# Kernel optimization log

Measured on AMD Instinct MI355X. Metric: run time of the kernel, lower is better.

The kernel has to match this reference:

```python
import jax, jax.numpy as jnp
import numpy as np
import math

NUM_CLASSES = 80
CENTER_RADIUS = 2.5
EPS = 1e-7
IMG = 1280.0


def _ciou(gt, pd):
    # gt: [G,4] xyxy, pd: [A,4] xyxy -> CIoU [G,A] (matches ultralytics bbox_iou, CIoU=True)
    b1 = gt[:, None, :]
    b2 = pd[None, :, :]
    iw = jnp.clip(jnp.minimum(b1[..., 2], b2[..., 2]) - jnp.maximum(b1[..., 0], b2[..., 0]), 0.0)
    ih = jnp.clip(jnp.minimum(b1[..., 3], b2[..., 3]) - jnp.maximum(b1[..., 1], b2[..., 1]), 0.0)
    inter = iw * ih
    w1 = b1[..., 2] - b1[..., 0]; h1 = b1[..., 3] - b1[..., 1]
    w2 = b2[..., 2] - b2[..., 0]; h2 = b2[..., 3] - b2[..., 1]
    union = w1 * h1 + w2 * h2 - inter + EPS
    iou = inter / union
    cw = jnp.maximum(b1[..., 2], b2[..., 2]) - jnp.minimum(b1[..., 0], b2[..., 0])
    ch = jnp.maximum(b1[..., 3], b2[..., 3]) - jnp.minimum(b1[..., 1], b2[..., 1])
    c2 = cw * cw + ch * ch + EPS
    rho2 = ((b2[..., 0] + b2[..., 2] - b1[..., 0] - b1[..., 2]) ** 2 +
            (b2[..., 1] + b2[..., 3] - b1[..., 1] - b1[..., 3]) ** 2) / 4.0
    v = (4.0 / math.pi ** 2) * (jnp.arctan(w2 / (h2 + EPS)) - jnp.arctan(w1 / (h1 + EPS))) ** 2
    alpha = v / (v - iou + (1.0 + EPS))
    return iou - (rho2 / c2 + v * alpha)


def _assign_one(scores, boxes, gt_lab, gt_box, valid, stride, anc):
    # scores [A,C], boxes [A,4], gt_lab [G], gt_box [G,4], valid [G] bool, stride [A,1], anc [A,2]
    G = gt_lab.shape[0]
    C = scores.shape[-1]
    # geometry constraint: anchor center within radius*stride of gt center
    gcx = (gt_box[:, 0] + gt_box[:, 2]) / 2.0
    gcy = (gt_box[:, 1] + gt_box[:, 3]) / 2.0
    cd = (stride[:, 0] * CENTER_RADIUS)[None, :]            # [1,A]
    in_center = (jnp.abs(anc[None, :, 0] - gcx[:, None]) < cd) & \
                (jnp.abs(anc[None, :, 1] - gcy[:, None]) < cd)
    in_center = in_center & valid[:, None]                  # [G,A]
    anchor_filter = in_center.any(axis=0)                   # [A]
    # pairwise CIoU (zeroed outside the filtered anchor set / invalid gts)
    ious = jnp.clip(_ciou(gt_box, boxes), 0.0)
    ious = ious * anchor_filter[None, :].astype(ious.dtype) * valid[:, None].astype(ious.dtype)
    iou_loss = -jnp.log(ious + 1e-8)
    # BCE(sqrt(p), onehot) summed over classes, computed without [G,A,C] tensor:
    # sum_c BCE = -sum_c log(1-p_c) - log p_{c_g} + log(1-p_{c_g})
    p = jnp.sqrt(scores)
    logp = jnp.clip(jnp.log(p), -100.0)
    log1mp = jnp.clip(jnp.log1p(-p), -100.0)
    base = -log1mp.sum(-1)                                  # [A]
    lp_g = jnp.take(logp, gt_lab, axis=1).T                 # [G,A]
    l1m_g = jnp.take(log1mp, gt_lab, axis=1).T              # [G,A]
    cls_loss = base[None, :] - lp_g + l1m_g
    # cost; extra 1e8/1e9 penalties emulate torch's exclusion of unfiltered anchors / invalid gts
    cost = (cls_loss + 3.0 * iou_loss
            + 1e6 * (~in_center).astype(cls_loss.dtype)
            + 1e8 * (~anchor_filter)[None, :].astype(cls_loss.dtype)
            + 1e9 * (~valid)[:, None].astype(cls_loss.dtype))
    # dynamic-k: sum of top-10 ious per gt
    topk_ious = jax.lax.top_k(ious, 10)[0]
    dyn_k = jnp.maximum((topk_ious.sum(-1) + 0.5).astype(jnp.int32), 1)
    # per-gt pick dyn_k lowest-cost anchors via rank
    ranks = jnp.argsort(jnp.argsort(cost, axis=-1), axis=-1)
    matching = (ranks < dyn_k[:, None]) & valid[:, None]    # [G,A] bool
    # conflict resolution: anchors matched to >1 gt keep min-cost gt
    cnt = matching.sum(0)                                   # [A]
    best_g = jnp.argmin(cost, axis=0)                       # [A]
    onehot_g = jnp.arange(G)[:, None] == best_g[None, :]
    matching = jnp.where(cnt[None, :] > 1, onehot_g, matching)
    fg = matching.any(axis=0)                               # [A]
    mg = jnp.argmax(matching, axis=0)                       # [A]
    pred_iou = (matching.astype(ious.dtype) * ious).sum(0)  # [A]
    labels = jnp.where(fg, gt_lab[mg], NUM_CLASSES).astype(jnp.int32)
    tboxes = gt_box[mg] * fg[:, None].astype(gt_box.dtype)
    tscores = jax.nn.one_hot(gt_lab[mg], C, dtype=scores.dtype) * (pred_iou * fg)[:, None]
    tgt_idx = jnp.where(fg, mg, 0).astype(jnp.int32)
    return labels, tboxes, tscores, fg, tgt_idx


def setup_inputs() -> dict:
    key = jax.random.key(0)
    ks = jax.random.split(key, 10)
    bs, A, G, C = 16, 33600, 64, NUM_CLASSES
    pd_scores = jax.random.uniform(ks[0], (bs, A, C), jnp.float32, 1e-4, 0.99)
    cxy = jax.random.uniform(ks[1], (bs, A, 2), jnp.float32, 0.0, IMG)
    wh = jax.random.uniform(ks[2], (bs, A, 2), jnp.float32, 8.0, 128.0)
    pd_bboxes = jnp.concatenate([cxy - wh / 2, cxy + wh / 2], axis=-1)
    anc_points = jax.random.uniform(ks[3], (A, 2), jnp.float32, 0.0, IMG)
    gt_labels = jax.random.randint(ks[4], (bs, G, 1), 0, C, jnp.int32)
    gcxy = jax.random.uniform(ks[5], (bs, G, 2), jnp.float32, 64.0, IMG - 64.0)
    gwh = jax.random.uniform(ks[6], (bs, G, 2), jnp.float32, 16.0, 256.0)
    gt_bboxes = jnp.concatenate([gcxy - gwh / 2, gcxy + gwh / 2], axis=-1)
    mask_gt = (jax.random.randint(ks[7], (bs, G, 1), 0, 5, jnp.int32) < 4).astype(jnp.int32)
    stride = (8.0 * (2.0 ** jax.random.randint(ks[8], (bs, A, 1), 0, 3, jnp.int32).astype(jnp.float32)))
    return {"pd_scores": pd_scores, "pd_bboxes": pd_bboxes, "anc_points": anc_points,
            "gt_labels": gt_labels, "gt_bboxes": gt_bboxes, "mask_gt": mask_gt, "stride": stride}


def reference(pd_scores, pd_bboxes, anc_points, gt_labels, gt_bboxes, mask_gt, stride):
    gt_lab = gt_labels[..., 0].astype(jnp.int32)
    valid = mask_gt[..., 0].astype(bool)
    fn = jax.vmap(_assign_one, in_axes=(0, 0, 0, 0, 0, 0, None))
    return fn(pd_scores, pd_bboxes, gt_lab, gt_bboxes, valid, stride, anc_points)
```

## Files before the change

kernel.cpp:

```cpp
#include <hip/hip_runtime.h>
#include <float.h>
#include <math.h>

#define NA 33600
#define NG 64
#define NC 80
#define NB 16
#define CRAD 2.5f
#define MCAP 12288

typedef float vfloat4 __attribute__((ext_vector_type(4)));

#define O_CNT   0ULL
#define O_AG    2150400ULL
#define O_AIOU  4300800ULL
#define O_BASE  6451200ULL
#define O_CCNT  8601600ULL
#define O_CONFC 8601664ULL
#define O_CONFL 8601728ULL
#define O_CA    8667264ULL
#define O_CBASE 9453696ULL
#define O_COLT  10240128ULL
#define WS_NEED_COLT (10240128ULL + 62914560ULL)
#define O_CPB   73154688ULL
#define O_CAP   76300416ULL
#define WS_NEED_PC (76300416ULL + 3145728ULL)
#define O_PIOU  79446144ULL
#define O_PCST  79528064ULL
#define O_PIDX  79609984ULL
#define O_CKEY  79773824ULL
#define WS_NEED_KEY (79773824ULL + 786432ULL)

#define OFF_LAB 0L
#define OFF_TB  537600L
#define OFF_TS  2688000L
#define OFF_FG  45696000L
#define OFF_TGT 46233600L
#define OUT_TOTAL 46771200L

__device__ __forceinline__ float ciou_clip(float gx1, float gy1, float gx2, float gy2,
                                           float w1, float h1, float at1, float at2v,
                                           float4 pb) {
    float iw = fmaxf(fminf(gx2, pb.z) - fmaxf(gx1, pb.x), 0.f);
    float ih = fmaxf(fminf(gy2, pb.w) - fmaxf(gy1, pb.y), 0.f);
    float inter = iw * ih;
    float w2 = pb.z - pb.x, h2 = pb.w - pb.y;
    float uni = w1 * h1 + w2 * h2 - inter + 1e-7f;
    float iou = inter / uni;
    float cw = fmaxf(gx2, pb.z) - fminf(gx1, pb.x);
    float ch = fmaxf(gy2, pb.w) - fminf(gy1, pb.y);
    float c2 = cw * cw + ch * ch + 1e-7f;
    float dx = pb.x + pb.z - gx1 - gx2;
    float dy = pb.y + pb.w - gy1 - gy2;
    float rho2 = (dx * dx + dy * dy) * 0.25f;
    float dat = at2v - at1;
    float v = 0.4052847345693511f * (dat * dat);
    float alpha = v / ((v - iou) + 1.0000001f);
    float ci = iou - (rho2 / c2 + v * alpha);
    return fmaxf(ci, 0.f);
}

__global__ __launch_bounds__(256) void k1a_cand(
    const float* __restrict__ anc, const float* __restrict__ gbox,
    const int* __restrict__ gmask, const float* __restrict__ strd,
    int* __restrict__ candA, unsigned int* __restrict__ candKey, int use_key,
    int* __restrict__ candCnt, int* __restrict__ cnt)
{
    __shared__ float2 s_c[NG];
    const int b = blockIdx.y, tid = threadIdx.x;
    if (tid < NG) {
        const float4 gb = ((const float4*)gbox)[b * NG + tid];
        const int v = gmask[b * NG + tid];
        float gcx = (gb.x + gb.z) * 0.5f;
        float gcy = (gb.y + gb.w) * 0.5f;
        s_c[tid] = make_float2(v ? gcx : 3.0e30f, gcy);
    }
    __syncthreads();
    const int a = blockIdx.x * 256 + tid;
    int f = 0;
    if (a < NA) {
        cnt[(long)b * NA + a] = 0;
        float2 ap = ((const float2*)anc)[a];
        float cd = strd[(long)b * NA + a] * CRAD;
        #pragma unroll
        for (int g = 0; g < NG; ++g) {
            float2 c = s_c[g];
            f |= (int)((fabsf(ap.x - c.x) < cd) & (fabsf(ap.y - c.y) < cd));
        }
    }
    unsigned long long m = __ballot(f);
    int lane = tid & 63;
    int wcnt = __popcll(m);
    int pre = __popcll(m & ((1ULL << lane) - 1ULL));
    int base0 = 0;
    if (lane == 0 && wcnt) base0 = atomicAdd(&candCnt[b], wcnt);
    base0 = __shfl(base0, 0, 64);
    if (f) {
        int pos = base0 + pre;
        if (pos < MCAP) {
            candA[b * MCAP + pos] = a;
            if (use_key) candKey[b * MCAP + pos] = ((unsigned int)a << 16) | (unsigned int)pos;
        }
    }
}

__global__ __launch_bounds__(256) void k1b_gather(
    const float* __restrict__ scores, const float* __restrict__ pdb,
    const float* __restrict__ anc, const float* __restrict__ strd,
    const int* __restrict__ candCnt, const int* __restrict__ candA,
    float* __restrict__ base, float* __restrict__ candBase,
    float* __restrict__ colT, int use_colT,
    float4* __restrict__ candPB, float4* __restrict__ candAp, int use_pc)
{
    __shared__ float s_l1m[64][81];
    const int b = blockIdx.y;
    int M = candCnt[b]; if (M > MCAP) M = MCAP;
    if (blockIdx.x * 64 >= M) return;
    const int q   = threadIdx.x >> 2;
    const int sub = threadIdx.x & 3;
    const int j = blockIdx.x * 64 + q;
    const bool active = (j < M);
    int a = 0;
    if (active) a = candA[b * MCAP + j];
    const long ia = (long)b * NA + a;
    if (active) {
        if (sub == 1 && use_pc) {
            float4 pb = ((const float4*)pdb)[ia];
            float2 ap = ((const float2*)anc)[a];
            float cd = strd[ia] * CRAD;
            float at2v = atanf((pb.z - pb.x) / ((pb.w - pb.y) + 1e-7f));
            candPB[b * MCAP + j] = pb;
            candAp[b * MCAP + j] = make_float4(ap.x, ap.y, cd, at2v);
        }
        const vfloat4* srow = (const vfloat4*)(scores + ia * NC);
        float* ct = colT + (long)b * NC * MCAP + j;
        #pragma unroll
        for (int qq = 0; qq < 5; ++qq) {
            vfloat4 s4 = __builtin_nontemporal_load(&srow[sub * 5 + qq]);
            float sv[4] = {s4.x, s4.y, s4.z, s4.w};
            #pragma unroll
            for (int k = 0; k < 4; ++k) {
                const int c = sub * 20 + 4 * qq + k;
                float p = sqrtf(sv[k]);
                float l1m = fmaxf(log1pf(-p), -100.f);
                s_l1m[q][c] = l1m;
                if (use_colT) {
                    float lp = fmaxf(logf(p), -100.f);
                    __builtin_nontemporal_store(l1m - lp, &ct[(long)c * MCAP]);
                }
            }
        }
    }
    __syncthreads();
    if (active && sub == 0) {
        float bsum = 0.f;
        #pragma unroll
        for (int c = 0; c < NC; ++c)
            bsum += s_l1m[q][c];
        const float bval = -bsum;
        base[ia] = bval;
        candBase[b * MCAP + j] = bval;
    }
}

__global__ __launch_bounds__(256) void k2_scan(
    const int* __restrict__ glab, const float* __restrict__ gbox,
    const int* __restrict__ gmask,
    const int* __restrict__ candCnt, const unsigned int* __restrict__ candKey,
    const float* __restrict__ candBase, const float* __restrict__ colT,
    const float4* __restrict__ candPB, const float4* __restrict__ candAp,
    float* __restrict__ partIou, float* __restrict__ partCost,
    unsigned int* __restrict__ partIdx)
{
    const int i = blockIdx.y;
    const int s = blockIdx.x;
    const int b = (i & 7) | ((i >> 9) << 3);
    const int g = (i >> 3) & 63;
    if (gmask[b * NG + g] == 0) return;
    const int tid = threadIdx.x, lane = tid & 63, wid = tid >> 6;
    __shared__ float s_v[4];
    __shared__ int s_i[4];
    __shared__ unsigned int s_u[4];

    const float4 gb = ((const float4*)gbox)[b * NG + g];
    const int lab = glab[b * NG + g];
    const float gcx = (gb.x + gb.z) * 0.5f, gcy = (gb.y + gb.w) * 0.5f;
    const float w1 = gb.z - gb.x, h1 = gb.w - gb.y;
    const float at1 = atanf(w1 / (h1 + 1e-7f));
    const int bM = b * MCAP;
    int M = candCnt[b]; if (M > MCAP) M = MCAP;
    const float* colrow = colT + (long)(b * NC + lab) * MCAP;

    float liou[10];
    float lcost[10]; unsigned int lkey[10];
    #pragma unroll
    for (int j = 0; j < 10; ++j) {
        liou[j] = 0.f;
        lcost[j] = FLT_MAX; lkey[j] = 0xFFFFFFFFu;
    }

    for (int jj = s * 256 + tid; jj < M; jj += 512) {
        const unsigned int key = candKey[bM + jj];
        const float4 pb = candPB[bM + jj];
        const float4 t  = candAp[bM + jj];
        const float cb  = candBase[bM + jj];
        const float cr  = colrow[jj];
        float ci = ciou_clip(gb.x, gb.y, gb.z, gb.w, w1, h1, at1, t.w, pb);
        bool inc = (fabsf(t.x - gcx) < t.z) && (fabsf(t.y - gcy) < t.z);
        float colv = cb + cr;
        float cost = colv + 3.0f * (-logf(ci + 1e-8f));
        if (!inc) cost += 1e6f;

        if (ci > liou[9]) {
            #pragma unroll
            for (int k = 9; k >= 1; --k) {
                bool ck   = (liou[k] > ci);
                bool ckm1 = (liou[k - 1] > ci);
                liou[k] = ck ? liou[k] : (ckm1 ? ci : liou[k - 1]);
            }
            liou[0] = (liou[0] > ci) ? liou[0] : ci;
        }
        if (cost < lcost[9] || (cost == lcost[9] && key < lkey[9])) {
            #pragma unroll
            for (int k = 9; k >= 1; --k) {
                bool ck   = (lcost[k] < cost) || (lcost[k] == cost && lkey[k] < key);
                bool ckm1 = (lcost[k - 1] < cost) || (lcost[k - 1] == cost && lkey[k - 1] < key);
                lcost[k] = ck ? lcost[k] : (ckm1 ? cost : lcost[k - 1]);
                lkey[k]  = ck ? lkey[k]  : (ckm1 ? key  : lkey[k - 1]);
            }
            bool c0 = (lcost[0] < cost) || (lcost[0] == cost && lkey[0] < key);
            lcost[0] = c0 ? lcost[0] : cost;
            lkey[0]  = c0 ? lkey[0]  : key;
        }
    }

    const int pbase = i * 20 + s * 10;
    for (int it = 0; it < 10; ++it) {
        float bv = liou[0];
        #pragma unroll
        for (int off = 32; off > 0; off >>= 1)
            bv = fmaxf(bv, __shfl_down(bv, off, 64));
        if (lane == 0) s_v[wid] = bv;
        __syncthreads();
        float wv = fmaxf(fmaxf(s_v[0], s_v[1]), fmaxf(s_v[2], s_v[3]));
        if (tid == 0) partIou[pbase + it] = wv;
        unsigned long long m = __ballot(liou[0] == wv);
        int fl = m ? (int)__ffsll((long long)m) - 1 : 64;
        if (lane == 0) s_i[wid] = fl;
        __syncthreads();
        int ow, ol;
        if (s_i[0] < 64)      { ow = 0; ol = s_i[0]; }
        else if (s_i[1] < 64) { ow = 1; ol = s_i[1]; }
        else if (s_i[2] < 64) { ow = 2; ol = s_i[2]; }
        else                  { ow = 3; ol = s_i[3]; }
        if (wid == ow && lane == ol) {
            #pragma unroll
            for (int k = 0; k < 9; ++k) liou[k] = liou[k + 1];
            liou[9] = -2.f;
        }
        __syncthreads();
    }
    for (int it = 0; it < 10; ++it) {
        float bc = lcost[0]; unsigned int bk = lkey[0];
        #pragma unroll
        for (int off = 32; off > 0; off >>= 1) {
            float oc = __shfl_down(bc, off, 64);
            unsigned int ok = __shfl_down(bk, off, 64);
            if (oc < bc || (oc == bc && ok < bk)) { bc = oc; bk = ok; }
        }
        if (lane == 0) { s_v[wid] = bc; s_u[wid] = bk; }
        __syncthreads();
        float wc = s_v[0]; unsigned int wk = s_u[0];
        #pragma unroll
        for (int w = 1; w < 4; ++w)
            if (s_v[w] < wc || (s_v[w] == wc && s_u[w] < wk)) { wc = s_v[w]; wk = s_u[w]; }
        if (lcost[0] == wc && lkey[0] == wk) {
            partCost[pbase + it] = wc;
            partIdx[pbase + it]  = wk;
            #pragma unroll
            for (int k = 0; k < 9; ++k) { lcost[k] = lcost[k + 1]; lkey[k] = lkey[k + 1]; }
            lcost[9] = FLT_MAX; lkey[9] = 0xFFFFFFFFu;
        }
        __syncthreads();
    }
}

__global__ __launch_bounds__(256) void k2b_merge(
    const int* __restrict__ gmask, const float* __restrict__ gbox,
    const float* __restrict__ partIou, const float* __restrict__ partCost,
    const unsigned int* __restrict__ partIdx,
    const float4* __restrict__ candPB, const float4* __restrict__ candAp,
    int* __restrict__ cnt, int* __restrict__ ag, float* __restrict__ aiou)
{
    const int lane = threadIdx.x & 63;
    const int wv0 = blockIdx.x * 4 + (threadIdx.x >> 6);
    for (int i = wv0; i < NB * NG; i += gridDim.x * 4) {
        const int b = (i & 7) | ((i >> 9) << 3);
        const int g = (i >> 3) & 63;
        if (gmask[b * NG + g] == 0) continue;
        float v = (lane < 20) ? partIou[i * 20 + lane] : -2.f;
        float acc = 0.f;
        for (int it = 0; it < 10; ++it) {
            float bv = v;
            #pragma unroll
            for (int off = 32; off > 0; off >>= 1)
                bv = fmaxf(bv, __shfl_down(bv, off, 64));
            bv = __shfl(bv, 0, 64);
            acc += bv;
            unsigned long long m = __ballot(v == bv);
            int first = (int)__ffsll((long long)m) - 1;
            if (lane == first) v = -3.f;
        }
        int K = (int)(acc + 0.5f);
        if (K < 1) K = 1;

        const float4 gbw = ((const float4*)gbox)[b * NG + g];
        const float w1w = gbw.z - gbw.x, h1w = gbw.w - gbw.y;
        const float at1w = atanf(w1w / (h1w + 1e-7f));
        const long bA = (long)b * NA;
        const int bM = b * MCAP;
        float c  = (lane < 20) ? partCost[i * 20 + lane] : FLT_MAX;
        unsigned int idx = (lane < 20) ? partIdx[i * 20 + lane] : 0xFFFFFFFFu;
        for (int it = 0; it < K; ++it) {
            float bc = c; unsigned int bk = idx;
            #pragma unroll
            for (int off = 32; off > 0; off >>= 1) {
                float oc = __shfl_down(bc, off, 64);
                unsigned int ok = __shfl_down(bk, off, 64);
                if (oc < bc || (oc == bc && ok < bk)) { bc = oc; bk = ok; }
            }
            bc = __shfl(bc, 0, 64);
            bk = (unsigned int)__shfl((int)bk, 0, 64);
            bool own = (c == bc && idx == bk);
            unsigned long long mo = __ballot(own);
            int fl = (int)__ffsll((long long)mo) - 1;
            if (own && lane == fl) {
                unsigned int aa = bk >> 16;
                if (aa < NA) {
                    int j = (int)(bk & 0xFFFFu);
                    float4 pbw = candPB[bM + j];
                    float4 tw  = candAp[bM + j];
                    float ciw = ciou_clip(gbw.x, gbw.y, gbw.z, gbw.w, w1w, h1w, at1w, tw.w, pbw);
                    atomicAdd(&cnt[bA + aa], 1);
                    ag[bA + aa] = g;
                    aiou[bA + aa] = ciw;
                }
            }
            if (own) { c = FLT_MAX; idx = 0xFFFFFFFFu; }
        }
    }
}

__global__ __launch_bounds__(256) void k2_select(
    const float* __restrict__ scores, const float* __restrict__ pdb,
    const float* __restrict__ anc, const int* __restrict__ glab,
    const float* __restrict__ gbox, const int* __restrict__ gmask,
    const float* __restrict__ strd,
    const int* __restrict__ candCnt, const int* __restrict__ candA,
    const float* __restrict__ candBase, const float* __restrict__ colT, int use_colT,
    const float4* __restrict__ candPB, const float4* __restrict__ candAp, int use_pc,
    int* __restrict__ cnt, int* __restrict__ ag, float* __restrict__ aiou)
{
    const int i = blockIdx.x;
    const int b = (i & 7) | ((i >> 9) << 3);
    const int g = (i >> 3) & 63;
    if (gmask[b * NG + g] == 0) return;
    const int tid = threadIdx.x, lane = tid & 63, wid = tid >> 6;
    __shared__ float s_v[4];
    __shared__ int s_i[4];

    const float4 gb = ((const float4*)gbox)[b * NG + g];
    const int lab = glab[b * NG + g];
    const float gcx = (gb.x + gb.z) * 0.5f, gcy = (gb.y + gb.w) * 0.5f;
    const float w1 = gb.z - gb.x, h1 = gb.w - gb.y;
    const float at1 = atanf(w1 / (h1 + 1e-7f));
    const long bA = (long)b * NA;
    const int bM = b * MCAP;
    int M = candCnt[b]; if (M > MCAP) M = MCAP;
    const float* colrow = colT + (long)(b * NC + lab) * MCAP;

    float liou[10]; int liodx[10];
    float lcost[10]; int lidx[10]; float lci[10];
    #pragma unroll
    for (int j = 0; j < 10; ++j) {
        liou[j] = 0.f;  liodx[j] = 0x40000000 + tid * 10 + j;
        lcost[j] = FLT_MAX; lidx[j] = 0x40000000 + tid * 10 + j; lci[j] = 0.f;
    }

    for (int jj = tid; jj < M; jj += 256) {
        const int a = candA[bM + jj];
        const long ia = bA + a;
        float4 pb; float apx, apy, cd, at2v;
        if (use_pc) {
            pb = candPB[bM + jj];
            float4 t = candAp[bM + jj];
            apx = t.x; apy = t.y; cd = t.z; at2v = t.w;
        } else {
            pb = ((const float4*)pdb)[ia];
            at2v = atanf((pb.z - pb.x) / ((pb.w - pb.y) + 1e-7f));
            float2 ap = ((const float2*)anc)[a];
            apx = ap.x; apy = ap.y;
            cd = strd[ia] * CRAD;
        }
        float ci = ciou_clip(gb.x, gb.y, gb.z, gb.w, w1, h1, at1, at2v, pb);
        bool inc = (fabsf(apx - gcx) < cd) && (fabsf(apy - gcy) < cd);
        float colv;
        if (use_colT) {
            colv = candBase[bM + jj] + colrow[jj];
        } else {
            float s = scores[ia * (long)NC + lab];
            float p = sqrtf(s);
            colv = candBase[bM + jj] + (fmaxf(log1pf(-p), -100.f) - fmaxf(logf(p), -100.f));
        }
        float cost = colv + 3.0f * (-logf(ci + 1e-8f));
        if (!inc) cost += 1e6f;

        if (ci > 0.f && (ci > liou[9] || (ci == liou[9] && a < liodx[9]))) {
            int p10 = 0;
            #pragma unroll
            for (int k = 0; k < 10; ++k)
                p10 += (liou[k] > ci || (liou[k] == ci && liodx[k] < a)) ? 1 : 0;
            #pragma unroll
            for (int j = 9; j >= 0; --j) {
                float pv = (j > 0) ? liou[j - 1] : 0.f;
                int pvi  = (j > 0) ? liodx[j - 1] : 0;
                bool sh = (j > p10), he = (j == p10);
                liou[j]  = sh ? pv  : (he ? ci : liou[j]);
                liodx[j] = sh ? pvi : (he ? a  : liodx[j]);
            }
        }
        if (cost < lcost[9] || (cost == lcost[9] && a < lidx[9])) {
            int p10 = 0;
            #pragma unroll
            for (int k = 0; k < 10; ++k)
                p10 += (lcost[k] < cost || (lcost[k] == cost && lidx[k] < a)) ? 1 : 0;
            #pragma unroll
            for (int j = 9; j >= 0; --j) {
                float pv = (j > 0) ? lcost[j - 1] : FLT_MAX;
                int pvi  = (j > 0) ? lidx[j - 1] : 0;
                float pvc = (j > 0) ? lci[j - 1] : 0.f;
                bool sh = (j > p10), he = (j == p10);
                lcost[j] = sh ? pv  : (he ? cost : lcost[j]);
                lidx[j]  = sh ? pvi : (he ? a    : lidx[j]);
                lci[j]   = sh ? pvc : (he ? ci   : lci[j]);
            }
        }
    }

    float acc = 0.f;
    for (int it = 0; it < 10; ++it) {
        float bv = -2.f; int bi = 0x7fffffff;
        #pragma unroll
        for (int j = 0; j < 10; ++j)
            if (liou[j] > bv || (liou[j] == bv && liodx[j] < bi)) { bv = liou[j]; bi = liodx[j]; }
        for (int off = 32; off > 0; off >>= 1) {
            float ov = __shfl_down(bv, off, 64);
            int   oi = __shfl_down(bi, off, 64);
            if (ov > bv || (ov == bv && oi < bi)) { bv = ov; bi = oi; }
        }
        if (lane == 0) { s_v[wid] = bv; s_i[wid] = bi; }
        __syncthreads();
        float wv = s_v[0]; int wi = s_i[0];
        #pragma unroll
        for (int w = 1; w < 4; ++w)
            if (s_v[w] > wv || (s_v[w] == wv && s_i[w] < wi)) { wv = s_v[w]; wi = s_i[w]; }
        acc += wv;
        #pragma unroll
        for (int j = 0; j < 10; ++j)
            if (liou[j] == wv && liodx[j] == wi) { liou[j] = -2.f; liodx[j] = 0x7fffffff; }
        __syncthreads();
    }
    int K = (int)(acc + 0.5f);
    if (K < 1) K = 1;

    for (int it = 0; it < K; ++it) {
        float bc = FLT_MAX; int bi = 0x7fffffff;
        #pragma unroll
        for (int j = 0; j < 10; ++j)
            if (lcost[j] < bc || (lcost[j] == bc && lidx[j] < bi)) { bc = lcost[j]; bi = lidx[j]; }
        for (int off = 32; off > 0; off >>= 1) {
            float oc = __shfl_down(bc, off, 64);
            int   oi = __shfl_down(bi, off, 64);
            if (oc < bc || (oc == bc && oi < bi)) { bc = oc; bi = oi; }
        }
        if (lane == 0) { s_v[wid] = bc; s_i[wid] = bi; }
        __syncthreads();
        float wc = s_v[0]; int wi = s_i[0];
        #pragma unroll
        for (int w = 1; w < 4; ++w)
            if (s_v[w] < wc || (s_v[w] == wc && s_i[w] < wi)) { wc = s_v[w]; wi = s_i[w]; }
        if (wi < NA) {
            #pragma unroll
            for (int j = 0; j < 10; ++j)
                if (lcost[j] == wc && lidx[j] == wi) {
                    atomicAdd(&cnt[bA + wi], 1);
                    ag[bA + wi] = g;
                    aiou[bA + wi] = lci[j];
                    lcost[j] = FLT_MAX; lidx[j] = 0x7fffffff;
                }
        }
        __syncthreads();
    }
}

__global__ __launch_bounds__(256) void k3_main(
    const int* __restrict__ glab, const float* __restrict__ gbox,
    const int* __restrict__ cnt, const int* __restrict__ ag, const float* __restrict__ aiou,
    int* __restrict__ confCnt, int* __restrict__ confList, float* __restrict__ out)
{
    const int tid = threadIdx.x;
    const long i = (long)blockIdx.x * 256 + tid;
    const int b = (int)(i / NA);
    const int c = cnt[i];
    float labo = 80.f;
    const bool conflict = (c > 1);
    if (c == 1) {
        int g = ag[i]; float iou = aiou[i];
        int lb = glab[b * NG + g];
        labo = (float)lb;
        ((float4*)(out + OFF_TB))[i] = ((const float4*)gbox)[b * NG + g];
        out[OFF_FG + i] = 1.f;
        out[OFF_TGT + i] = (float)g;
        out[OFF_TS + i * NC + lb] = iou;
    }
    unsigned long long m = __ballot(conflict ? 1 : 0);
    int lane = tid & 63;
    int wcnt = __popcll(m);
    int pre = __popcll(m & ((1ULL << lane) - 1ULL));
    int base0 = 0;
    if (lane == 0 && wcnt) base0 = atomicAdd(confCnt, wcnt);
    base0 = __shfl(base0, 0, 64);
    if (conflict) confList[base0 + pre] = (int)i;
    else out[OFF_LAB + i] = labo;
}

__global__ __launch_bounds__(256) void k3b_conflict(
    const float* __restrict__ scores, const float* __restrict__ pdb,
    const float* __restrict__ anc, const int* __restrict__ glab,
    const float* __restrict__ gbox, const int* __restrict__ gmask,
    const float* __restrict__ strd, const float* __restrict__ base,
    const int* __restrict__ confCnt, const int* __restrict__ confList,
    float* __restrict__ out)
{
    const int lane = threadIdx.x & 63;
    const int waveId = blockIdx.x * 4 + (threadIdx.x >> 6);
    const int nWaves = gridDim.x * 4;
    int n = *confCnt; if (n > 16384) n = 16384;
    for (int idx = waveId; idx < n; idx += nWaves) {
        const long i = (long)confList[idx];
        const int b = (int)(i / NA); const int a = (int)(i % NA);
        const int g = lane;
        float4 pb = ((const float4*)pdb)[i];
        float bse = base[i];
        float at2v = atanf((pb.z - pb.x) / ((pb.w - pb.y) + 1e-7f));
        float2 ap = ((const float2*)anc)[a];
        float cd = strd[i] * CRAD;
        float cost = FLT_MAX; float iom = 0.f;
        if (gmask[b * NG + g] != 0) {
            float4 gb = ((const float4*)gbox)[b * NG + g];
            float w1 = gb.z - gb.x, h1 = gb.w - gb.y;
            float at1 = atanf(w1 / (h1 + 1e-7f));
            iom = ciou_clip(gb.x, gb.y, gb.z, gb.w, w1, h1, at1, at2v, pb);
            float gcx = (gb.x + gb.z) * 0.5f, gcy = (gb.y + gb.w) * 0.5f;
            bool inc = (fabsf(ap.x - gcx) < cd) && (fabsf(ap.y - gcy) < cd);
            int lb = glab[b * NG + g];
            float s = scores[i * (long)NC + lb];
            float p = sqrtf(s);
            float clsv = bse + (fmaxf(log1pf(-p), -100.f) - fmaxf(logf(p), -100.f));
            cost = clsv + 3.0f * (-logf(iom + 1e-8f));
            if (!inc) cost += 1e6f;
        }
        float bc = cost; int bg = g; float bio = iom;
        for (int off = 32; off > 0; off >>= 1) {
            float oc = __shfl_down(bc, off, 64);
            int   og = __shfl_down(bg, off, 64);
            float oo = __shfl_down(bio, off, 64);
            if (oc < bc || (oc == bc && og < bg)) { bc = oc; bg = og; bio = oo; }
        }
        if (lane == 0) {
            int lb = glab[b * NG + bg];
            out[OFF_LAB + i] = (float)lb;
            ((float4*)(out + OFF_TB))[i] = ((const float4*)gbox)[b * NG + bg];
            out[OFF_FG + i] = 1.f;
            out[OFF_TGT + i] = (float)bg;
            out[OFF_TS + i * NC + lb] = bio;
        }
    }
}

extern "C" void kernel_launch(void* const* d_in, const int* in_sizes, int n_in,
                              void* d_out, int out_size, void* d_ws, size_t ws_size,
                              hipStream_t stream) {
    const float* scores = (const float*)d_in[0];
    const float* pdb    = (const float*)d_in[1];
    const float* anc    = (const float*)d_in[2];
    const int*   glab   = (const int*)d_in[3];
    const float* gbox   = (const float*)d_in[4];
    const int*   gmask  = (const int*)d_in[5];
    const float* strd   = (const float*)d_in[6];
    float* out = (float*)d_out;
    char* ws = (char*)d_ws;

    int*    cnt      = (int*)(ws + O_CNT);
    int*    ag       = (int*)(ws + O_AG);
    float*  aiou     = (float*)(ws + O_AIOU);
    float*  base     = (float*)(ws + O_BASE);
    int*    candCnt  = (int*)(ws + O_CCNT);
    int*    confCnt  = (int*)(ws + O_CONFC);
    int*    confList = (int*)(ws + O_CONFL);
    int*    candA    = (int*)(ws + O_CA);
    float*  candBase = (float*)(ws + O_CBASE);
    float*  colT     = (float*)(ws + O_COLT);
    float4* candPB   = (float4*)(ws + O_CPB);
    float4* candAp   = (float4*)(ws + O_CAP);
    float*  partIou  = (float*)(ws + O_PIOU);
    float*  partCost = (float*)(ws + O_PCST);
    unsigned int* partIdx = (unsigned int*)(ws + O_PIDX);
    unsigned int* candKey = (unsigned int*)(ws + O_CKEY);
    const int use_colT  = (ws_size >= WS_NEED_COLT) ? 1 : 0;
    const int use_pc    = (ws_size >= WS_NEED_PC) ? 1 : 0;
    const int use_split = (ws_size >= WS_NEED_KEY && use_colT && use_pc) ? 1 : 0;

    (void)hipMemsetAsync(out + OFF_TB, 0, (size_t)(OUT_TOTAL - OFF_TB) * sizeof(float), stream);
    (void)hipMemsetAsync(candCnt, 0, 128, stream);
    k1a_cand<<<dim3((NA + 255) / 256, NB), 256, 0, stream>>>(
        anc, gbox, gmask, strd, candA, candKey, use_split, candCnt, cnt);
    k1b_gather<<<dim3((MCAP + 63) / 64, NB), 256, 0, stream>>>(
        scores, pdb, anc, strd, candCnt, candA, base, candBase, colT, use_colT,
        candPB, candAp, use_pc);
    if (use_split) {
        k2_scan<<<dim3(2, NB * NG), 256, 0, stream>>>(
            glab, gbox, gmask, candCnt, candKey, candBase, colT, candPB, candAp,
            partIou, partCost, partIdx);
        k2b_merge<<<64, 256, 0, stream>>>(
            gmask, gbox, partIou, partCost, partIdx, candPB, candAp, cnt, ag, aiou);
    } else {
        k2_select<<<NB * NG, 256, 0, stream>>>(
            scores, pdb, anc, glab, gbox, gmask, strd,
            candCnt, candA, candBase, colT, use_colT, candPB, candAp, use_pc,
            cnt, ag, aiou);
    }
    k3_main<<<(NB * NA) / 256, 256, 0, stream>>>(
        glab, gbox, cnt, ag, aiou, confCnt, confList, out);
    k3b_conflict<<<128, 256, 0, stream>>>(
        scores, pdb, anc, glab, gbox, gmask, strd, base,
        confCnt, confList, out);
}
```

Baseline: 571.2 us.

## Build per-GT in-center candidate lists and split top-k IoU from cost selection

The candidate kernel now records, for each anchor, a bitmask of the GTs whose center region contains it, and appends the anchor key to a per-GT list of up to 512 entries using atomics. A new k2_iou kernel computes the dynamic k from the top-10 CIoU over all candidates, and k2_cost does the cost top-k scan over only that GT's in-center list (one wavefront per GT). This replaces the split scan/merge path so the cost scan no longer walks every candidate per GT. The price is extra atomics in k1a, an added kernel launch, and a fallback full scan when a list overflows or holds fewer than 10 entries.

```diff
diff --git a/kernel.cpp b/kernel.cpp
--- a/kernel.cpp
+++ b/kernel.cpp
@@ -8,6 +8,7 @@
 #define NB 16
 #define CRAD 2.5f
 #define MCAP 12288
+#define CAPG 512
 
 typedef float vfloat4 __attribute__((ext_vector_type(4)));
 
@@ -30,6 +31,11 @@
 #define O_PIDX  79609984ULL
 #define O_CKEY  79773824ULL
 #define WS_NEED_KEY (79773824ULL + 786432ULL)
+#define O_LCNT  80560256ULL
+#define O_KARR  80564352ULL
+#define O_GTL   80568448ULL
+#define O_CAT   82665600ULL
+#define WS_NEED_NEW (82665600ULL + 786432ULL)
 
 #define OFF_LAB 0L
 #define OFF_TB  537600L
@@ -64,6 +70,7 @@
     const float* __restrict__ anc, const float* __restrict__ gbox,
     const int* __restrict__ gmask, const float* __restrict__ strd,
     int* __restrict__ candA, unsigned int* __restrict__ candKey, int use_key,
+    int* __restrict__ listCnt, int* __restrict__ gtList, int use_new,
     int* __restrict__ candCnt, int* __restrict__ cnt)
 {
     __shared__ float2 s_c[NG];
@@ -77,7 +84,7 @@
     }
     __syncthreads();
     const int a = blockIdx.x * 256 + tid;
-    int f = 0;
+    unsigned long long hit = 0ULL;
     if (a < NA) {
         cnt[(long)b * NA + a] = 0;
         float2 ap = ((const float2*)anc)[a];
@@ -85,9 +92,12 @@
         #pragma unroll
         for (int g = 0; g < NG; ++g) {
             float2 c = s_c[g];
-            f |= (int)((fabsf(ap.x - c.x) < cd) & (fabsf(ap.y - c.y) < cd));
-        }
-    }
+            unsigned long long in =
+                (unsigned long long)((fabsf(ap.x - c.x) < cd) & (fabsf(ap.y - c.y) < cd));
+            hit |= in << g;
+        }
+    }
+    int f = (hit != 0ULL) ? 1 : 0;
     unsigned long long m = __ballot(f);
     int lane = tid & 63;
     int wcnt = __popcll(m);
@@ -99,7 +109,17 @@
         int pos = base0 + pre;
         if (pos < MCAP) {
             candA[b * MCAP + pos] = a;
-            if (use_key) candKey[b * MCAP + pos] = ((unsigned int)a << 16) | (unsigned int)pos;
+            unsigned int key = ((unsigned int)a << 16) | (unsigned int)pos;
+            if (use_key) candKey[b * MCAP + pos] = key;
+            if (use_new) {
+                unsigned long long m2 = hit;
+                while (m2) {
+                    int g = (int)__ffsll((long long)m2) - 1;
+                    m2 &= m2 - 1ULL;
+                    int lp = atomicAdd(&listCnt[b * NG + g], 1);
+                    if (lp < CAPG) gtList[(b * NG + g) * CAPG + lp] = (int)key;
+                }
+            }
         }
     }
 }
@@ -110,7 +130,8 @@
     const int* __restrict__ candCnt, const int* __restrict__ candA,
     float* __restrict__ base, float* __restrict__ candBase,
     float* __restrict__ colT, int use_colT,
-    float4* __restrict__ candPB, float4* __restrict__ candAp, int use_pc)
+    float4* __restrict__ candPB, float4* __restrict__ candAp, int use_pc,
+    float* __restrict__ candAt, int use_new)
 {
     __shared__ float s_l1m[64][81];
     const int b = blockIdx.y;
@@ -131,6 +152,7 @@
             float at2v = atanf((pb.z - pb.x) / ((pb.w - pb.y) + 1e-7f));
             candPB[b * MCAP + j] = pb;
             candAp[b * MCAP + j] = make_float4(ap.x, ap.y, cd, at2v);
+            if (use_new) candAt[b * MCAP + j] = at2v;
         }
         const vfloat4* srow = (const vfloat4*)(scores + ia * NC);
         float* ct = colT + (long)b * NC * MCAP + j;
@@ -160,6 +182,189 @@
         const float bval = -bsum;
         base[ia] = bval;
         candBase[b * MCAP + j] = bval;
+    }
+}
+
+__global__ __launch_bounds__(256) void k2_iou(
+    const float* __restrict__ gbox, const int* __restrict__ gmask,
+    const int* __restrict__ candCnt,
+    const float4* __restrict__ candPB, const float* __restrict__ candAt,
+    int* __restrict__ kArr)
+{
+    const int i = blockIdx.x;
+    const int b = (i & 7) | ((i >> 9) << 3);
+    const int g = (i >> 3) & 63;
+    if (gmask[b * NG + g] == 0) return;
+    const int tid = threadIdx.x, lane = tid & 63, wid = tid >> 6;
+    __shared__ float s_v[4];
+    __shared__ int s_i[4];
+
+    const float4 gb = ((const float4*)gbox)[b * NG + g];
+    const float w1 = gb.z - gb.x, h1 = gb.w - gb.y;
+    const float at1 = atanf(w1 / (h1 + 1e-7f));
+    const int bM = b * MCAP;
+    int M = candCnt[b]; if (M > MCAP) M = MCAP;
+
+    float liou[10];
+    #pragma unroll
+    for (int j = 0; j < 10; ++j) liou[j] = 0.f;
+
+    for (int jj = tid; jj < M; jj += 256) {
+        float4 pb = candPB[bM + jj];
+        float at2v = candAt[bM + jj];
+        float ci = ciou_clip(gb.x, gb.y, gb.z, gb.w, w1, h1, at1, at2v, pb);
+        if (ci > liou[9]) {
+            #pragma unroll
+            for (int k = 9; k >= 1; --k) {
+                bool ck   = (liou[k] > ci);
+                bool ckm1 = (liou[k - 1] > ci);
+                liou[k] = ck ? liou[k] : (ckm1 ? ci : liou[k - 1]);
+            }
+            liou[0] = (liou[0] > ci) ? liou[0] : ci;
+        }
+    }
+
+    float acc = 0.f;
+    for (int it = 0; it < 10; ++it) {
+        float bv = liou[0];
+        #pragma unroll
+        for (int off = 32; off > 0; off >>= 1)
+            bv = fmaxf(bv, __shfl_down(bv, off, 64));
+        if (lane == 0) s_v[wid] = bv;
+        __syncthreads();
+        float wv = fmaxf(fmaxf(s_v[0], s_v[1]), fmaxf(s_v[2], s_v[3]));
+        acc += wv;
+        unsigned long long m = __ballot(liou[0] == wv);
+        int fl = m ? (int)__ffsll((long long)m) - 1 : 64;
+        if (lane == 0) s_i[wid] = fl;
+        __syncthreads();
+        int ow, ol;
+        if (s_i[0] < 64)      { ow = 0; ol = s_i[0]; }
+        else if (s_i[1] < 64) { ow = 1; ol = s_i[1]; }
+        else if (s_i[2] < 64) { ow = 2; ol = s_i[2]; }
+        else                  { ow = 3; ol = s_i[3]; }
+        if (wid == ow && lane == ol) {
+            #pragma unroll
+            for (int k = 0; k < 9; ++k) liou[k] = liou[k + 1];
+            liou[9] = -2.f;
+        }
+        __syncthreads();
+    }
+    if (tid == 0) {
+        int K = (int)(acc + 0.5f);
+        if (K < 1) K = 1;
+        kArr[i] = K;
+    }
+}
+
+__global__ __launch_bounds__(256) void k2_cost(
+    const int* __restrict__ glab, const float* __restrict__ gbox,
+    const int* __restrict__ gmask,
+    const int* __restrict__ candCnt, const int* __restrict__ candA,
+    const float* __restrict__ candBase, const float* __restrict__ colT,
+    const float4* __restrict__ candPB, const float4* __restrict__ candAp,
+    const float* __restrict__ candAt,
+    const int* __restrict__ listCnt, const int* __restrict__ gtList,
+    const int* __restrict__ kArr,
+    int* __restrict__ cnt, int* __restrict__ ag, float* __restrict__ aiou)
+{
+    const int lane = threadIdx.x & 63;
+    const int i = blockIdx.x * 4 + (threadIdx.x >> 6);
+    if (i >= NB * NG) return;
+    const int b = (i & 7) | ((i >> 9) << 3);
+    const int g = (i >> 3) & 63;
+    if (gmask[b * NG + g] == 0) return;
+    const int K = kArr[i];
+
+    const float4 gb = ((const float4*)gbox)[b * NG + g];
+    const int lab = glab[b * NG + g];
+    const float w1 = gb.z - gb.x, h1 = gb.w - gb.y;
+    const float at1 = atanf(w1 / (h1 + 1e-7f));
+    const long bA = (long)b * NA;
+    const int bM = b * MCAP;
+    const float* colrow = colT + (long)(b * NC + lab) * MCAP;
+
+    float lcost[10]; unsigned int lkey[10]; float lci[10];
+    #pragma unroll
+    for (int j = 0; j < 10; ++j) { lcost[j] = FLT_MAX; lkey[j] = 0xFFFFFFFFu; lci[j] = 0.f; }
+
+    const int C = listCnt[b * NG + g];
+    if (C >= 10 && C <= CAPG) {
+        const int* lst = gtList + (b * NG + g) * CAPG;
+        for (int t = lane; t < C; t += 64) {
+            const unsigned int key = (unsigned int)lst[t];
+            const int j = (int)(key & 0xFFFFu);
+            float4 pb = candPB[bM + j];
+            float at2v = candAt[bM + j];
+            float ci = ciou_clip(gb.x, gb.y, gb.z, gb.w, w1, h1, at1, at2v, pb);
+            float colv = candBase[bM + j] + colrow[j];
+            float cost = colv + 3.0f * (-logf(ci + 1e-8f));
+            if (cost < lcost[9] || (cost == lcost[9] && key < lkey[9])) {
+                #pragma unroll
+                for (int k = 9; k >= 1; --k) {
+                    bool ck   = (lcost[k] < cost) || (lcost[k] == cost && lkey[k] < key);
+                    bool ckm1 = (lcost[k - 1] < cost) || (lcost[k - 1] == cost && lkey[k - 1] < key);
+                    lcost[k] = ck ? lcost[k] : (ckm1 ? cost : lcost[k - 1]);
+                    lkey[k]  = ck ? lkey[k]  : (ckm1 ? key  : lkey[k - 1]);
+                    lci[k]   = ck ? lci[k]   : (ckm1 ? ci   : lci[k - 1]);
+                }
+                bool c0 = (lcost[0] < cost) || (lcost[0] == cost && lkey[0] < key);
+                lcost[0] = c0 ? lcost[0] : cost;
+                lkey[0]  = c0 ? lkey[0]  : key;
+                lci[0]   = c0 ? lci[0]   : ci;
+            }
+        }
+    } else {
+        int M = candCnt[b]; if (M > MCAP) M = MCAP;
+        const float gcx = (gb.x + gb.z) * 0.5f, gcy = (gb.y + gb.w) * 0.5f;
+        for (int jj = lane; jj < M; jj += 64) {
+            const int a = candA[bM + jj];
+            const unsigned int key = ((unsigned int)a << 16) | (unsigned int)jj;
+            float4 pb = candPB[bM + jj];
+            float4 t  = candAp[bM + jj];
+            float ci = ciou_clip(gb.x, gb.y, gb.z, gb.w, w1, h1, at1, t.w, pb);
+            bool inc = (fabsf(t.x - gcx) < t.z) && (fabsf(t.y - gcy) < t.z);
+            float colv = candBase[bM + jj] + colrow[jj];
+            float cost = colv + 3.0f * (-logf(ci + 1e-8f));
+            if (!inc) cost += 1e6f;
+            if (cost < lcost[9] || (cost == lcost[9] && key < lkey[9])) {
+                #pragma unroll
+                for (int k = 9; k >= 1; --k) {
+                    bool ck   = (lcost[k] < cost) || (lcost[k] == cost && lkey[k] < key);
+                    bool ckm1 = (lcost[k - 1] < cost) || (lcost[k - 1] == cost && lkey[k - 1] < key);
+                    lcost[k] = ck ? lcost[k] : (ckm1 ? cost : lcost[k - 1]);
+                    lkey[k]  = ck ? lkey[k]  : (ckm1 ? key  : lkey[k - 1]);
+                    lci[k]   = ck ? lci[k]   : (ckm1 ? ci   : lci[k - 1]);
+                }
+                bool c0 = (lcost[0] < cost) || (lcost[0] == cost && lkey[0] < key);
+                lcost[0] = c0 ? lcost[0] : cost;
+                lkey[0]  = c0 ? lkey[0]  : key;
+                lci[0]   = c0 ? lci[0]   : ci;
+            }
+        }
+    }
+
+    for (int it = 0; it < K; ++it) {
+        float bc = lcost[0]; unsigned int bk = lkey[0];
+        #pragma unroll
+        for (int off = 32; off > 0; off >>= 1) {
+            float oc = __shfl_down(bc, off, 64);
+            unsigned int ok = __shfl_down(bk, off, 64);
+            if (oc < bc || (oc == bc && ok < bk)) { bc = oc; bk = ok; }
+        }
+        bc = __shfl(bc, 0, 64);
+        bk = (unsigned int)__shfl((int)bk, 0, 64);
+        if (lcost[0] == bc && lkey[0] == bk) {
+            unsigned int aa = bk >> 16;
+            if (aa < NA) {
+                atomicAdd(&cnt[bA + aa], 1);
+                ag[bA + aa] = g;
+                aiou[bA + aa] = lci[0];
+            }
+            #pragma unroll
+            for (int k = 0; k < 9; ++k) { lcost[k] = lcost[k + 1]; lkey[k] = lkey[k + 1]; lci[k] = lci[k + 1]; }
+            lcost[9] = FLT_MAX; lkey[9] = 0xFFFFFFFFu; lci[9] = 0.f;
+        }
     }
 }
 
@@ -617,18 +822,31 @@
     float*  partCost = (float*)(ws + O_PCST);
     unsigned int* partIdx = (unsigned int*)(ws + O_PIDX);
     unsigned int* candKey = (unsigned int*)(ws + O_CKEY);
+    int*    listCnt  = (int*)(ws + O_LCNT);
+    int*    kArr     = (int*)(ws + O_KARR);
+    int*    gtList   = (int*)(ws + O_GTL);
+    float*  candAt   = (float*)(ws + O_CAT);
     const int use_colT  = (ws_size >= WS_NEED_COLT) ? 1 : 0;
     const int use_pc    = (ws_size >= WS_NEED_PC) ? 1 : 0;
-    const int use_split = (ws_size >= WS_NEED_KEY && use_colT && use_pc) ? 1 : 0;
+    const int use_new   = (ws_size >= WS_NEED_NEW && use_colT && use_pc) ? 1 : 0;
+    const int use_split = (!use_new && ws_size >= WS_NEED_KEY && use_colT && use_pc) ? 1 : 0;
 
     (void)hipMemsetAsync(out + OFF_TB, 0, (size_t)(OUT_TOTAL - OFF_TB) * sizeof(float), stream);
     (void)hipMemsetAsync(candCnt, 0, 128, stream);
+    if (use_new) (void)hipMemsetAsync(listCnt, 0, 4096, stream);
     k1a_cand<<<dim3((NA + 255) / 256, NB), 256, 0, stream>>>(
-        anc, gbox, gmask, strd, candA, candKey, use_split, candCnt, cnt);
+        anc, gbox, gmask, strd, candA, candKey, use_split,
+        listCnt, gtList, use_new, candCnt, cnt);
     k1b_gather<<<dim3((MCAP + 63) / 64, NB), 256, 0, stream>>>(
         scores, pdb, anc, strd, candCnt, candA, base, candBase, colT, use_colT,
-        candPB, candAp, use_pc);
-    if (use_split) {
+        candPB, candAp, use_pc, candAt, use_new);
+    if (use_new) {
+        k2_iou<<<NB * NG, 256, 0, stream>>>(
+            gbox, gmask, candCnt, candPB, candAt, kArr);
+        k2_cost<<<NB * NG / 4, 256, 0, stream>>>(
+            glab, gbox, gmask, candCnt, candA, candBase, colT,
+            candPB, candAp, candAt, listCnt, gtList, kArr, cnt, ag, aiou);
+    } else if (use_split) {
         k2_scan<<<dim3(2, NB * NG), 256, 0, stream>>>(
             glab, gbox, gmask, candCnt, candKey, candBase, colT, candPB, candAp,
             partIou, partCost, partIdx);
```

Measured after the change: 536.3 us. 6.1% less time.
